# Kernel tuning notes

Hardware: AMD Instinct MI355X
Metric: run time of the kernel (lower is better)

Reference implementation:

```python
import jax, jax.numpy as jnp
import numpy as np

N = 50000      # nodes
E = 800000     # edges
F_IN = 256     # feature_dim
H = 128        # inter_dim
D = 64         # embd_dim
MAX_LOGSTD = 10.0
LEAKY_SLOPE = 0.01


def _lin_params(key, fan_in, fan_out):
    kw, kb = jax.random.split(key)
    s = 1.0 / np.sqrt(fan_in)
    W = jax.random.uniform(kw, (fan_in, fan_out), minval=-s, maxval=s, dtype=jnp.float32)
    b = jax.random.uniform(kb, (fan_out,), minval=-s, maxval=s, dtype=jnp.float32)
    return W, b


def setup_inputs() -> dict:
    key = jax.random.key(0)
    ks = jax.random.split(key, 12)
    x = jax.random.normal(ks[0], (N, F_IN), dtype=jnp.float32)
    edge_index = jax.random.randint(ks[1], (2, E), 0, N, dtype=jnp.int64)
    W_gcn, b_gcn = _lin_params(ks[2], F_IN, H)
    Wq_mu, bq_mu = _lin_params(ks[3], H, D)
    Wk_mu, bk_mu = _lin_params(ks[4], H, D)
    Wv_mu, bv_mu = _lin_params(ks[5], H, D)
    Ws_mu, bs_mu = _lin_params(ks[6], H, D)
    Wq_ls, bq_ls = _lin_params(ks[7], H, D)
    Wk_ls, bk_ls = _lin_params(ks[8], H, D)
    Wv_ls, bv_ls = _lin_params(ks[9], H, D)
    Ws_ls, bs_ls = _lin_params(ks[10], H, D)
    return dict(x=x, edge_index=edge_index, W_gcn=W_gcn, b_gcn=b_gcn,
                Wq_mu=Wq_mu, bq_mu=bq_mu, Wk_mu=Wk_mu, bk_mu=bk_mu,
                Wv_mu=Wv_mu, bv_mu=bv_mu, Ws_mu=Ws_mu, bs_mu=bs_mu,
                Wq_ls=Wq_ls, bq_ls=bq_ls, Wk_ls=Wk_ls, bk_ls=bk_ls,
                Wv_ls=Wv_ls, bv_ls=bv_ls, Ws_ls=Ws_ls, bs_ls=bs_ls)


def gcn_conv(x, src, dst, W, b, n):
    # PyG GCNConv: h = xW; add self loops; norm = d^-1/2[src]*d^-1/2[dst]; scatter-add to dst; + b
    h = x @ W
    loop = jnp.arange(n, dtype=src.dtype)
    src2 = jnp.concatenate([src, loop])
    dst2 = jnp.concatenate([dst, loop])
    deg = jax.ops.segment_sum(jnp.ones_like(dst2, dtype=h.dtype), dst2, num_segments=n)
    dinv = jnp.where(deg > 0, jax.lax.rsqrt(deg), 0.0)
    norm = dinv[src2] * dinv[dst2]                       # [E+N]
    out = jax.ops.segment_sum(h[src2] * norm[:, None], dst2, num_segments=n)
    return out + b


def transformer_conv(x, src, dst, Wq, bq, Wk, bk, Wv, bv, Ws, bs, n):
    # PyG TransformerConv, heads=1, concat=True, beta=False, root_weight=True
    c = Wq.shape[1]
    q = x @ Wq + bq
    k = x @ Wk + bk
    v = x @ Wv + bv
    alpha = jnp.sum(q[dst] * k[src], axis=-1) / jnp.sqrt(jnp.asarray(c, x.dtype))  # [E]
    amax = jax.ops.segment_max(alpha, dst, num_segments=n)
    ex = jnp.exp(alpha - amax[dst])
    denom = jax.ops.segment_sum(ex, dst, num_segments=n)
    w = ex / (denom[dst] + 1e-16)                        # scatter softmax over edges per dst
    out = jax.ops.segment_sum(v[src] * w[:, None], dst, num_segments=n)
    return out + (x @ Ws + bs)


def reference(x, edge_index, W_gcn, b_gcn,
              Wq_mu, bq_mu, Wk_mu, bk_mu, Wv_mu, bv_mu, Ws_mu, bs_mu,
              Wq_ls, bq_ls, Wk_ls, bk_ls, Wv_ls, bv_ls, Ws_ls, bs_ls):
    n = x.shape[0]
    src, dst = edge_index[0], edge_index[1]
    h = gcn_conv(x, src, dst, W_gcn, b_gcn, n)
    h = jnp.where(h >= 0, h, LEAKY_SLOPE * h)            # LeakyReLU(0.01)
    mu = transformer_conv(h, src, dst, Wq_mu, bq_mu, Wk_mu, bk_mu, Wv_mu, bv_mu, Ws_mu, bs_mu, n)
    logstd = transformer_conv(h, src, dst, Wq_ls, bq_ls, Wk_ls, bk_ls, Wv_ls, bv_ls, Ws_ls, bs_ls, n)
    logstd = jnp.minimum(logstd, MAX_LOGSTD)
    return mu, logstd
```

## Files before the change

### kernel.cpp

```cpp
#include <hip/hip_runtime.h>
#include <math.h>

#define N_NODES 50000
#define N_EDGES 800000
#define F_IN    256
#define H_DIM   128
#define D_DIM   64
#define MAX_LOGSTD 10.0f
#define LEAKY_SLOPE 0.01f

#define NB       196
#define BCAP     5000
#define GEMM_BLK 782

using bf16x8 = __attribute__((ext_vector_type(8))) short;
using f32x4  = __attribute__((ext_vector_type(4))) float;

__device__ inline float bflo(unsigned u) { return __uint_as_float(u << 16); }
__device__ inline float bfhi(unsigned u) { return __uint_as_float(u & 0xFFFF0000u); }
__device__ inline unsigned short f2bf(float f) {
    unsigned u = __float_as_uint(f);
    u += 0x7FFFu + ((u >> 16) & 1u);
    return (unsigned short)(u >> 16);
}
__device__ inline unsigned pack2(float a, float b) {
    return (unsigned)f2bf(a) | ((unsigned)f2bf(b) << 16);
}

__global__ void k_prep(const float* __restrict__ Wg,
                       const float* __restrict__ Wq0, const float* __restrict__ Wk0,
                       const float* __restrict__ Wv0, const float* __restrict__ Ws0,
                       const float* __restrict__ Wq1, const float* __restrict__ Wk1,
                       const float* __restrict__ Wv1, const float* __restrict__ Ws1,
                       unsigned short* __restrict__ wfg, unsigned short* __restrict__ wfm,
                       unsigned short* __restrict__ wfl, int* __restrict__ gCursor) {
    int blk = blockIdx.x, t = threadIdx.x;
    if (blk == 384) { if (t < 256) gCursor[t] = 0; return; }
    int grp = blk >> 7;
    int tid = (blk & 127) * 256 + t;
    if (grp == 0) {
        int j = tid & 7, ct = (tid >> 3) & 1, ks = (tid >> 4) & 7;
        int l = (tid >> 7) & 63, w = tid >> 13;
        int k = ks * 32 + (l >> 4) * 8 + j;
        int n = w * 32 + ct * 16 + (l & 15);
        wfg[tid] = f2bf(Wg[k * H_DIM + n]);
    } else {
        int j = tid & 7, ct = (tid >> 3) & 3, ks = (tid >> 5) & 3;
        int l = (tid >> 7) & 63, w = tid >> 13;
        int k = ks * 32 + (l >> 4) * 8 + j;
        int n = ct * 16 + (l & 15);
        const float* Wsrc = (grp == 1)
            ? ((w == 0) ? Wq0 : (w == 1) ? Wk0 : (w == 2) ? Wv0 : Ws0)
            : ((w == 0) ? Wq1 : (w == 1) ? Wk1 : (w == 2) ? Wv1 : Ws1);
        unsigned short val = f2bf(Wsrc[k * D_DIM + n]);
        if (grp == 1) wfm[tid] = val; else wfl[tid] = val;
    }
}

__global__ __launch_bounds__(256) void k_bucketA(
        const int* __restrict__ src, const int* __restrict__ dst,
        int* __restrict__ gCursor, uint2* __restrict__ staging) {
    __shared__ int cnt[NB];
    __shared__ int base[NB];
    int t = threadIdx.x;
    int e0 = blockIdx.x * 4096;
    for (int i = t; i < NB; i += 256) cnt[i] = 0;
    __syncthreads();
    int s[16], d[16], b[16];
#pragma unroll
    for (int i = 0; i < 16; ++i) {
        int e = e0 + t + i * 256;
        if (e < N_EDGES) {
            s[i] = src[e]; d[i] = dst[e]; b[i] = d[i] >> 8;
            atomicAdd(&cnt[b[i]], 1);
        } else b[i] = -1;
    }
    __syncthreads();
    for (int i = t; i < NB; i += 256) base[i] = atomicAdd(&gCursor[i], cnt[i]);
    __syncthreads();
    for (int i = t; i < NB; i += 256) cnt[i] = 0;
    __syncthreads();
#pragma unroll
    for (int i = 0; i < 16; ++i) {
        if (b[i] >= 0) {
            int lp = atomicAdd(&cnt[b[i]], 1);
            staging[(size_t)b[i] * BCAP + base[b[i]] + lp] =
                make_uint2((unsigned)s[i], (unsigned)d[i]);
        }
    }
}

__global__ __launch_bounds__(256) void k_bucketB(
        const uint2* __restrict__ staging, const int* __restrict__ gCursor,
        int* __restrict__ rowptr, float* __restrict__ dinv, int* __restrict__ srcs) {
    __shared__ int sg[256];
    __shared__ int dcnt[256], doff[256], dcur[256];
    int b = blockIdx.x, t = threadIdx.x;
    sg[t] = (t < NB) ? gCursor[t] : 0;
    dcnt[t] = 0;
    __syncthreads();
    int n = sg[b];
    for (int off = 1; off < 256; off <<= 1) {
        int u = (t >= off) ? sg[t - off] : 0;
        __syncthreads();
        sg[t] += u;
        __syncthreads();
    }
    int bb = sg[b] - n;
// ... 47 lines not shown
        float4 a1 = xg[(size_t)grow * 64 + c16 * 2 + 1];
        uint4 o;
        o.x = pack2(a0.x, a0.y); o.y = pack2(a0.z, a0.w);
        o.z = pack2(a1.x, a1.y); o.w = pack2(a1.z, a1.w);
        sA[row * 32 + (c16 ^ (row & 7))] = o;
    }
    __syncthreads();
    f32x4 zero = {0.f, 0.f, 0.f, 0.f};
    f32x4 acc[4][2];
#pragma unroll
    for (int rt = 0; rt < 4; ++rt) { acc[rt][0] = zero; acc[rt][1] = zero; }
    int lr = l & 15, lh = l >> 4;
#pragma unroll
    for (int ks = 0; ks < 8; ++ks) {
        bf16x8 a[4];
#pragma unroll
        for (int rt = 0; rt < 4; ++rt) {
            int row = rt * 16 + lr;
            int c4 = (ks * 4 + lh) ^ (row & 7);
            a[rt] = ((const bf16x8*)sA)[row * 32 + c4];
        }
#pragma unroll
        for (int rt = 0; rt < 4; ++rt) {
            acc[rt][0] = __builtin_amdgcn_mfma_f32_16x16x32_bf16(a[rt], bfr[ks][0], acc[rt][0], 0, 0, 0);
            acc[rt][1] = __builtin_amdgcn_mfma_f32_16x16x32_bf16(a[rt], bfr[ks][1], acc[rt][1], 0, 0, 0);
        }
    }
#pragma unroll
    for (int rt = 0; rt < 4; ++rt)
#pragma unroll
        for (int j = 0; j < 4; ++j) {
            int row = r0 + rt * 16 + lh * 4 + j;
            if (row < N_NODES) {
                float dv = dinv[row];
                size_t base = (size_t)row * H_DIM + w * 32 + lr;
                h0b[base]      = f2bf(acc[rt][0][j] * dv);
                h0b[base + 16] = f2bf(acc[rt][1][j] * dv);
            }
        }
}

__global__ void k_gcn_gather(const unsigned short* __restrict__ h0b,
                             const int* __restrict__ rowptr, const int* __restrict__ srcs,
                             const float* __restrict__ dinv, const float* __restrict__ b,
                             unsigned short* __restrict__ hb) {
    int t = threadIdx.x;
    int node = blockIdx.x * 16 + (t >> 4);
    int sl = t & 15;
    if (node >= N_NODES) return;
    uint4 U = ((const uint4*)(h0b + (size_t)node * H_DIM))[sl];
    float acc[8] = {bflo(U.x), bfhi(U.x), bflo(U.y), bfhi(U.y),
                    bflo(U.z), bfhi(U.z), bflo(U.w), bfhi(U.w)};
    int beg = rowptr[node], end = rowptr[node + 1];
    for (int p = beg; p < end; ++p) {
        int s = srcs[p];
        uint4 V = ((const uint4*)(h0b + (size_t)s * H_DIM))[sl];
        acc[0] += bflo(V.x); acc[1] += bfhi(V.x);
        acc[2] += bflo(V.y); acc[3] += bfhi(V.y);
        acc[4] += bflo(V.z); acc[5] += bfhi(V.z);
        acc[6] += bflo(V.w); acc[7] += bfhi(V.w);
    }
    float dv = dinv[node];
    float out[8];
#pragma unroll
    for (int i = 0; i < 8; ++i) {
        float val = acc[i] * dv + b[sl * 8 + i];
        out[i] = (val >= 0.f) ? val : LEAKY_SLOPE * val;
    }
    uint4 o;
    o.x = pack2(out[0], out[1]); o.y = pack2(out[2], out[3]);
    o.z = pack2(out[4], out[5]); o.w = pack2(out[6], out[7]);
    ((uint4*)(hb + (size_t)node * H_DIM))[sl] = o;
}

__global__ __launch_bounds__(256) void k_qkvs_mfma(
        const unsigned short* __restrict__ hb, const unsigned short* __restrict__ wfrag,
        const float* __restrict__ bq, const float* __restrict__ bk,
        const float* __restrict__ bv, const float* __restrict__ bs,
        float* __restrict__ q, unsigned short* __restrict__ kvb,
        float* __restrict__ outp) {
    __shared__ uint4 sA[64 * 16];
    int t = threadIdx.x, l = t & 63, w = t >> 6;
    int r0 = blockIdx.x * 64;
    const bf16x8* Wf = ((const bf16x8*)wfrag) + ((w * 64 + l) << 4);
    bf16x8 bfr[4][4];
#pragma unroll
    for (int ks = 0; ks < 4; ++ks)
#pragma unroll
        for (int ct = 0; ct < 4; ++ct) bfr[ks][ct] = Wf[ks * 4 + ct];
    const uint4* hg = (const uint4*)hb;
#pragma unroll
    for (int p = 0; p < 4; ++p) {
        int idx = t + p * 256;
        int row = idx >> 4, c16 = idx & 15;
        int grow = min(r0 + row, N_NODES - 1);
        sA[row * 16 + (c16 ^ (row & 7))] = hg[(size_t)grow * 16 + c16];
    }
    __syncthreads();
    f32x4 zero = {0.f, 0.f, 0.f, 0.f};
    f32x4 acc[4][4];
#pragma unroll
    for (int rt = 0; rt < 4; ++rt)
#pragma unroll
        for (int ct = 0; ct < 4; ++ct) acc[rt][ct] = zero;
    int lr = l & 15, lh = l >> 4;
#pragma unroll
    for (int ks = 0; ks < 4; ++ks) {
        bf16x8 a[4];
#pragma unroll
        for (int rt = 0; rt < 4; ++rt) {
            int row = rt * 16 + lr;
            int c4 = (ks * 4 + lh) ^ (row & 7);
            a[rt] = ((const bf16x8*)sA)[row * 16 + c4];
        }
#pragma unroll
        for (int rt = 0; rt < 4; ++rt)
#pragma unroll
            for (int ct = 0; ct < 4; ++ct)
                acc[rt][ct] = __builtin_amdgcn_mfma_f32_16x16x32_bf16(a[rt], bfr[ks][ct], acc[rt][ct], 0, 0, 0);
    }
    const float* bias = (w == 0) ? bq : (w == 1) ? bk : (w == 2) ? bv : bs;
    float bcol[4];
#pragma unroll
    for (int ct = 0; ct < 4; ++ct) bcol[ct] = bias[ct * 16 + lr];
#pragma unroll
    for (int rt = 0; rt < 4; ++rt)
#pragma unroll
        for (int j = 0; j < 4; ++j) {
            int row = r0 + rt * 16 + lh * 4 + j;
            if (row >= N_NODES) continue;
            float v0 = acc[rt][0][j] + bcol[0];
            float v1 = acc[rt][1][j] + bcol[1];
            float v2 = acc[rt][2][j] + bcol[2];
            float v3 = acc[rt][3][j] + bcol[3];
            if (w == 0) {
                float* qp = q + (size_t)row * D_DIM + lr;
                qp[0] = v0; qp[16] = v1; qp[32] = v2; qp[48] = v3;
            } else if (w == 1) {
                unsigned short* kp = kvb + (size_t)row * 128 + lr;
                kp[0] = f2bf(v0); kp[16] = f2bf(v1); kp[32] = f2bf(v2); kp[48] = f2bf(v3);
            } else if (w == 2) {
                unsigned short* vp = kvb + (size_t)row * 128 + 64 + lr;
                vp[0] = f2bf(v0); vp[16] = f2bf(v1); vp[32] = f2bf(v2); vp[48] = f2bf(v3);
            } else {
                float* op = outp + (size_t)row * D_DIM + lr;
                op[0] = v0; op[16] = v1; op[32] = v2; op[48] = v3;
            }
        }
}

__global__ void k_attn2(const float* __restrict__ qm, const float* __restrict__ ql,
                        const unsigned short* __restrict__ kvm, const unsigned short* __restrict__ kvl,
                        const int* __restrict__ rowptr, const int* __restrict__ srcs,
                        float* __restrict__ mu_out, float* __restrict__ ls_out) {
    int t = threadIdx.x;
    int node = blockIdx.x * 4 + (t >> 6);
    if (node >= N_NODES) return;
    int l = t & 63, g = l >> 4, sl = l & 15;
    float4 qm4 = ((const float4*)(qm + (size_t)node * D_DIM))[sl];
    float4 ql4 = ((const float4*)(ql + (size_t)node * D_DIM))[sl];
    qm4.x *= 0.125f; qm4.y *= 0.125f; qm4.z *= 0.125f; qm4.w *= 0.125f;
    ql4.x *= 0.125f; ql4.y *= 0.125f; ql4.z *= 0.125f; ql4.w *= 0.125f;
    int beg = rowptr[node], end = rowptr[node + 1];
    int deg = end - beg;
    int p0 = beg + ((deg * g) >> 2);
    int p1 = beg + ((deg * (g + 1)) >> 2);
    float m_m = -INFINITY, den_m = 0.f;
    float m_l = -INFINITY, den_l = 0.f;
    float4 am = make_float4(0.f, 0.f, 0.f, 0.f);
    float4 al = make_float4(0.f, 0.f, 0.f, 0.f);
    for (int p = p0; p < p1; ++p) {
        int s = srcs[p];
        const unsigned short* km = kvm + (size_t)s * 128;
        const unsigned short* kl = kvl + (size_t)s * 128;
        uint2 kum = *(const uint2*)(km + sl * 4);
        uint2 vum = *(const uint2*)(km + 64 + sl * 4);
        uint2 kul = *(const uint2*)(kl + sl * 4);
        uint2 vul = *(const uint2*)(kl + 64 + sl * 4);
        float dm = qm4.x * bflo(kum.x);
        dm = fmaf(qm4.y, bfhi(kum.x), dm);
        dm = fmaf(qm4.z, bflo(kum.y), dm);
        dm = fmaf(qm4.w, bfhi(kum.y), dm);
        float dl = ql4.x * bflo(kul.x);
        dl = fmaf(ql4.y, bfhi(kul.x), dl);
        dl = fmaf(ql4.z, bflo(kul.y), dl);
        dl = fmaf(ql4.w, bfhi(kul.y), dl);
        dm += __shfl_xor(dm, 1); dm += __shfl_xor(dm, 2);
        dm += __shfl_xor(dm, 4); dm += __shfl_xor(dm, 8);
        dl += __shfl_xor(dl, 1); dl += __shfl_xor(dl, 2);
        dl += __shfl_xor(dl, 4); dl += __shfl_xor(dl, 8);
        if (dm <= m_m) {
            float ex = __expf(dm - m_m);
            den_m += ex;
            am.x = fmaf(ex, bflo(vum.x), am.x);
            am.y = fmaf(ex, bfhi(vum.x), am.y);
            am.z = fmaf(ex, bflo(vum.y), am.z);
            am.w = fmaf(ex, bfhi(vum.y), am.w);
        } else {
            float sc = __expf(m_m - dm);
            den_m = fmaf(den_m, sc, 1.f);
            am.x = fmaf(am.x, sc, bflo(vum.x));
            am.y = fmaf(am.y, sc, bfhi(vum.x));
            am.z = fmaf(am.z, sc, bflo(vum.y));
            am.w = fmaf(am.w, sc, bfhi(vum.y));
            m_m = dm;
        }
        if (dl <= m_l) {
            float ex = __expf(dl - m_l);
            den_l += ex;
            al.x = fmaf(ex, bflo(vul.x), al.x);
            al.y = fmaf(ex, bfhi(vul.x), al.y);
            al.z = fmaf(ex, bflo(vul.y), al.z);
            al.w = fmaf(ex, bfhi(vul.y), al.w);
        } else {
            float sc = __expf(m_l - dl);
            den_l = fmaf(den_l, sc, 1.f);
            al.x = fmaf(al.x, sc, bflo(vul.x));
            al.y = fmaf(al.y, sc, bfhi(vul.x));
            al.z = fmaf(al.z, sc, bflo(vul.y));
            al.w = fmaf(al.w, sc, bfhi(vul.y));
            m_l = dl;
        }
    }
    float M = m_m;
    M = fmaxf(M, __shfl_xor(M, 16)); M = fmaxf(M, __shfl_xor(M, 32));
    float sc = (m_m == -INFINITY) ? 0.f : __expf(m_m - M);
    den_m *= sc; am.x *= sc; am.y *= sc; am.z *= sc; am.w *= sc;
    den_m += __shfl_xor(den_m, 16); den_m += __shfl_xor(den_m, 32);
    am.x += __shfl_xor(am.x, 16); am.x += __shfl_xor(am.x, 32);
    am.y += __shfl_xor(am.y, 16); am.y += __shfl_xor(am.y, 32);
    am.z += __shfl_xor(am.z, 16); am.z += __shfl_xor(am.z, 32);
    am.w += __shfl_xor(am.w, 16); am.w += __shfl_xor(am.w, 32);

    float L = m_l;
    L = fmaxf(L, __shfl_xor(L, 16)); L = fmaxf(L, __shfl_xor(L, 32));
    float scl = (m_l == -INFINITY) ? 0.f : __expf(m_l - L);
    den_l *= scl; al.x *= scl; al.y *= scl; al.z *= scl; al.w *= scl;
    den_l += __shfl_xor(den_l, 16); den_l += __shfl_xor(den_l, 32);
    al.x += __shfl_xor(al.x, 16); al.x += __shfl_xor(al.x, 32);
    al.y += __shfl_xor(al.y, 16); al.y += __shfl_xor(al.y, 32);
    al.z += __shfl_xor(al.z, 16); al.z += __shfl_xor(al.z, 32);
    al.w += __shfl_xor(al.w, 16); al.w += __shfl_xor(al.w, 32);

    if (g == 0) {
        float inv = 1.f / (den_m + 1e-16f);
        float4 sk = ((float4*)mu_out)[node * 16 + sl];
        float4 o = make_float4(am.x * inv + sk.x, am.y * inv + sk.y,
                               am.z * inv + sk.z, am.w * inv + sk.w);
        ((float4*)mu_out)[node * 16 + sl] = o;
        float invl = 1.f / (den_l + 1e-16f);
        float4 skl = ((float4*)ls_out)[node * 16 + sl];
        float4 ol = make_float4(al.x * invl + skl.x, al.y * invl + skl.y,
                                al.z * invl + skl.z, al.w * invl + skl.w);
        ol.x = fminf(ol.x, MAX_LOGSTD); ol.y = fminf(ol.y, MAX_LOGSTD);
        ol.z = fminf(ol.z, MAX_LOGSTD); ol.w = fminf(ol.w, MAX_LOGSTD);
        ((float4*)ls_out)[node * 16 + sl] = ol;
    }
}

extern "C" void kernel_launch(void* const* d_in, const int* in_sizes, int n_in,
                              void* d_out, int out_size, void* d_ws, size_t ws_size,
                              hipStream_t stream) {
    const float* x     = (const float*)d_in[0];
    const int*   ei    = (const int*)d_in[1];
    const int*   src   = ei;
    const int*   dst   = ei + N_EDGES;
    const float* W_gcn = (const float*)d_in[2];
    const float* b_gcn = (const float*)d_in[3];
    const float* Wm[8]; const float* Wl8[8];
    for (int i = 0; i < 8; ++i) { Wm[i] = (const float*)d_in[4 + i]; Wl8[i] = (const float*)d_in[12 + i]; }

    float* out    = (float*)d_out;
    float* mu_out = out;
    float* ls_out = out + N_NODES * D_DIM;

    float* ws   = (float*)d_ws;
    float* q_l  = ws;
    float* dinv = q_l + (size_t)N_NODES * D_DIM;
    unsigned short* kvm = (unsigned short*)(dinv + N_NODES);
    unsigned short* h0b = kvm + (size_t)N_NODES * H_DIM;
    unsigned short* hb  = h0b + (size_t)N_NODES * H_DIM;
    unsigned short* wfg = hb + (size_t)N_NODES * H_DIM;
    unsigned short* wfm = wfg + 32768;
    unsigned short* wfl = wfm + 32768;
    int* rowptr  = (int*)(wfl + 32768);
    int* srcs    = rowptr + N_NODES + 4;
    int* gCursor = srcs + N_EDGES;
    uint2* staging = (uint2*)(gCursor + 256);
    float* q_m     = (float*)staging;

    const int B = 256;
    k_prep<<<385, B, 0, stream>>>(W_gcn, Wm[0], Wm[2], Wm[4], Wm[6],
                                  Wl8[0], Wl8[2], Wl8[4], Wl8[6],
                                  wfg, wfm, wfl, gCursor);
    k_bucketA<<<(N_EDGES + 4095) / 4096, B, 0, stream>>>(src, dst, gCursor, staging);
    k_bucketB<<<NB, B, 0, stream>>>(staging, gCursor, rowptr, dinv, srcs);

    k_gemm_gcn_mfma<<<GEMM_BLK, B, 0, stream>>>(x, wfg, dinv, h0b);
    k_gcn_gather<<<(N_NODES + 15) / 16, B, 0, stream>>>(h0b, rowptr, srcs, dinv, b_gcn, hb);

    unsigned short* kvl = h0b;
    k_qkvs_mfma<<<GEMM_BLK, B, 0, stream>>>(hb, wfm, Wm[1], Wm[3], Wm[5], Wm[7],
                                            q_m, kvm, mu_out);
    k_qkvs_mfma<<<GEMM_BLK, B, 0, stream>>>(hb, wfl, Wl8[1], Wl8[3], Wl8[5], Wl8[7],
                                            q_l, kvl, ls_out);
    k_attn2<<<(N_NODES + 3) / 4, B, 0, stream>>>(q_m, q_l, kvm, kvl, rowptr, srcs,
                                                 mu_out, ls_out);
}
```

Baseline: 226.6 us.

## Fuse mu/logstd QKVS GEMMs into one launch and unroll gather loops by two

The two per-conv QKVS MFMA GEMM launches become a single 512-thread kernel. Its eight waves cover both convolutions, so each 64-row tile of h is loaded into shared memory once instead of twice. The GCN gather loop and the attention edge loop are unrolled by two so that more independent gather loads are in flight per iteration. The cost is higher register pressure in the attention kernel and larger blocks in the fused GEMM.

```diff
diff --git a/kernel.cpp b/kernel.cpp
--- a/kernel.cpp
+++ b/kernel.cpp
@@ -25,6 +25,36 @@
 }
 __device__ inline unsigned pack2(float a, float b) {
     return (unsigned)f2bf(a) | ((unsigned)f2bf(b) << 16);
+}
+__device__ inline float dot4(const float4& q, uint2 ku) {
+    float d = q.x * bflo(ku.x);
+    d = fmaf(q.y, bfhi(ku.x), d);
+    d = fmaf(q.z, bflo(ku.y), d);
+    d = fmaf(q.w, bfhi(ku.y), d);
+    return d;
+}
+__device__ inline float red16(float d) {
+    d += __shfl_xor(d, 1); d += __shfl_xor(d, 2);
+    d += __shfl_xor(d, 4); d += __shfl_xor(d, 8);
+    return d;
+}
+__device__ inline void sm_step(float d, uint2 vu, float& m, float& den, float4& a) {
+    if (d <= m) {
+        float ex = __expf(d - m);
+        den += ex;
+        a.x = fmaf(ex, bflo(vu.x), a.x);
+        a.y = fmaf(ex, bfhi(vu.x), a.y);
+        a.z = fmaf(ex, bflo(vu.y), a.z);
+        a.w = fmaf(ex, bfhi(vu.y), a.w);
+    } else {
+        float sc = __expf(m - d);
+        den = fmaf(den, sc, 1.f);
+        a.x = fmaf(a.x, sc, bflo(vu.x));
+        a.y = fmaf(a.y, sc, bfhi(vu.x));
+        a.z = fmaf(a.z, sc, bflo(vu.y));
+        a.w = fmaf(a.w, sc, bfhi(vu.y));
+        m = d;
+    }
 }
 
 __global__ void k_prep(const float* __restrict__ Wg,
@@ -207,7 +237,21 @@
     float acc[8] = {bflo(U.x), bfhi(U.x), bflo(U.y), bfhi(U.y),
                     bflo(U.z), bfhi(U.z), bflo(U.w), bfhi(U.w)};
     int beg = rowptr[node], end = rowptr[node + 1];
-    for (int p = beg; p < end; ++p) {
+    int p = beg;
+    for (; p + 1 < end; p += 2) {
+        int s0 = srcs[p], s1 = srcs[p + 1];
+        uint4 V0 = ((const uint4*)(h0b + (size_t)s0 * H_DIM))[sl];
+        uint4 V1 = ((const uint4*)(h0b + (size_t)s1 * H_DIM))[sl];
+        acc[0] += bflo(V0.x); acc[1] += bfhi(V0.x);
+        acc[2] += bflo(V0.y); acc[3] += bfhi(V0.y);
+        acc[4] += bflo(V0.z); acc[5] += bfhi(V0.z);
+        acc[6] += bflo(V0.w); acc[7] += bfhi(V0.w);
+        acc[0] += bflo(V1.x); acc[1] += bfhi(V1.x);
+        acc[2] += bflo(V1.y); acc[3] += bfhi(V1.y);
+        acc[4] += bflo(V1.z); acc[5] += bfhi(V1.z);
+        acc[6] += bflo(V1.w); acc[7] += bfhi(V1.w);
+    }
+    if (p < end) {
         int s = srcs[p];
         uint4 V = ((const uint4*)(h0b + (size_t)s * H_DIM))[sl];
         acc[0] += bflo(V.x); acc[1] += bfhi(V.x);
@@ -228,16 +272,21 @@
     ((uint4*)(hb + (size_t)node * H_DIM))[sl] = o;
 }
 
-__global__ __launch_bounds__(256) void k_qkvs_mfma(
-        const unsigned short* __restrict__ hb, const unsigned short* __restrict__ wfrag,
-        const float* __restrict__ bq, const float* __restrict__ bk,
-        const float* __restrict__ bv, const float* __restrict__ bs,
-        float* __restrict__ q, unsigned short* __restrict__ kvb,
-        float* __restrict__ outp) {
+__global__ __launch_bounds__(512) void k_qkvs2_mfma(
+        const unsigned short* __restrict__ hb,
+        const unsigned short* __restrict__ wfm, const unsigned short* __restrict__ wfl,
+        const float* __restrict__ bq0, const float* __restrict__ bk0,
+        const float* __restrict__ bv0, const float* __restrict__ bs0,
+        const float* __restrict__ bq1, const float* __restrict__ bk1,
+        const float* __restrict__ bv1, const float* __restrict__ bs1,
+        float* __restrict__ qm, unsigned short* __restrict__ kvm, float* __restrict__ mu_out,
+        float* __restrict__ ql, unsigned short* __restrict__ kvl, float* __restrict__ ls_out) {
     __shared__ uint4 sA[64 * 16];
     int t = threadIdx.x, l = t & 63, w = t >> 6;
+    int conv = w >> 2, role = w & 3;
     int r0 = blockIdx.x * 64;
-    const bf16x8* Wf = ((const bf16x8*)wfrag) + ((w * 64 + l) << 4);
+    const unsigned short* wfrag = conv ? wfl : wfm;
+    const bf16x8* Wf = ((const bf16x8*)wfrag) + ((role * 64 + l) << 4);
     bf16x8 bfr[4][4];
 #pragma unroll
     for (int ks = 0; ks < 4; ++ks)
@@ -245,8 +294,8 @@
         for (int ct = 0; ct < 4; ++ct) bfr[ks][ct] = Wf[ks * 4 + ct];
     const uint4* hg = (const uint4*)hb;
 #pragma unroll
-    for (int p = 0; p < 4; ++p) {
-        int idx = t + p * 256;
+    for (int p = 0; p < 2; ++p) {
+        int idx = t + p * 512;
         int row = idx >> 4, c16 = idx & 15;
         int grow = min(r0 + row, N_NODES - 1);
         sA[row * 16 + (c16 ^ (row & 7))] = hg[(size_t)grow * 16 + c16];
@@ -274,7 +323,12 @@
             for (int ct = 0; ct < 4; ++ct)
                 acc[rt][ct] = __builtin_amdgcn_mfma_f32_16x16x32_bf16(a[rt], bfr[ks][ct], acc[rt][ct], 0, 0, 0);
     }
-    const float* bias = (w == 0) ? bq : (w == 1) ? bk : (w == 2) ? bv : bs;
+    const float* bias = conv
+        ? ((role == 0) ? bq1 : (role == 1) ? bk1 : (role == 2) ? bv1 : bs1)
+        : ((role == 0) ? bq0 : (role == 1) ? bk0 : (role == 2) ? bv0 : bs0);
+    float* qp_   = conv ? ql : qm;
+    unsigned short* kvp_ = conv ? kvl : kvm;
+    float* op_   = conv ? ls_out : mu_out;
     float bcol[4];
 #pragma unroll
     for (int ct = 0; ct < 4; ++ct) bcol[ct] = bias[ct * 16 + lr];
@@ -288,17 +342,17 @@
             float v1 = acc[rt][1][j] + bcol[1];
             float v2 = acc[rt][2][j] + bcol[2];
             float v3 = acc[rt][3][j] + bcol[3];
-            if (w == 0) {
-                float* qp = q + (size_t)row * D_DIM + lr;
+            if (role == 0) {
+                float* qp = qp_ + (size_t)row * D_DIM + lr;
                 qp[0] = v0; qp[16] = v1; qp[32] = v2; qp[48] = v3;
-            } else if (w == 1) {
-                unsigned short* kp = kvb + (size_t)row * 128 + lr;
+            } else if (role == 1) {
+                unsigned short* kp = kvp_ + (size_t)row * 128 + lr;
                 kp[0] = f2bf(v0); kp[16] = f2bf(v1); kp[32] = f2bf(v2); kp[48] = f2bf(v3);
-            } else if (w == 2) {
-                unsigned short* vp = kvb + (size_t)row * 128 + 64 + lr;
+            } else if (role == 2) {
+                unsigned short* vp = kvp_ + (size_t)row * 128 + 64 + lr;
                 vp[0] = f2bf(v0); vp[16] = f2bf(v1); vp[32] = f2bf(v2); vp[48] = f2bf(v3);
             } else {
-                float* op = outp + (size_t)row * D_DIM + lr;
+                float* op = op_ + (size_t)row * D_DIM + lr;
                 op[0] = v0; op[16] = v1; op[32] = v2; op[48] = v3;
             }
         }
@@ -324,7 +378,31 @@
     float m_l = -INFINITY, den_l = 0.f;
     float4 am = make_float4(0.f, 0.f, 0.f, 0.f);
     float4 al = make_float4(0.f, 0.f, 0.f, 0.f);
-    for (int p = p0; p < p1; ++p) {
+    int p = p0;
+    for (; p + 1 < p1; p += 2) {
+        int s0 = srcs[p], s1 = srcs[p + 1];
+        const unsigned short* km0 = kvm + (size_t)s0 * 128;
+        const unsigned short* kl0 = kvl + (size_t)s0 * 128;
+        const unsigned short* km1 = kvm + (size_t)s1 * 128;
+        const unsigned short* kl1 = kvl + (size_t)s1 * 128;
+        uint2 kum0 = *(const uint2*)(km0 + sl * 4);
+        uint2 vum0 = *(const uint2*)(km0 + 64 + sl * 4);
+        uint2 kul0 = *(const uint2*)(kl0 + sl * 4);
+        uint2 vul0 = *(const uint2*)(kl0 + 64 + sl * 4);
+        uint2 kum1 = *(const uint2*)(km1 + sl * 4);
+        uint2 vum1 = *(const uint2*)(km1 + 64 + sl * 4);
+        uint2 kul1 = *(const uint2*)(kl1 + sl * 4);
+        uint2 vul1 = *(const uint2*)(kl1 + 64 + sl * 4);
+        float dm0 = red16(dot4(qm4, kum0));
+        float dl0 = red16(dot4(ql4, kul0));
+        float dm1 = red16(dot4(qm4, kum1));
+        float dl1 = red16(dot4(ql4, kul1));
+        sm_step(dm0, vum0, m_m, den_m, am);
+        sm_step(dm1, vum1, m_m, den_m, am);
+        sm_step(dl0, vul0, m_l, den_l, al);
+        sm_step(dl1, vul1, m_l, den_l, al);
+    }
+    if (p < p1) {
         int s = srcs[p];
         const unsigned short* km = kvm + (size_t)s * 128;
         const unsigned short* kl = kvl + (size_t)s * 128;
@@ -332,50 +410,10 @@
         uint2 vum = *(const uint2*)(km + 64 + sl * 4);
         uint2 kul = *(const uint2*)(kl + sl * 4);
         uint2 vul = *(const uint2*)(kl + 64 + sl * 4);
-        float dm = qm4.x * bflo(kum.x);
-        dm = fmaf(qm4.y, bfhi(kum.x), dm);
-        dm = fmaf(qm4.z, bflo(kum.y), dm);
-        dm = fmaf(qm4.w, bfhi(kum.y), dm);
-        float dl = ql4.x * bflo(kul.x);
-        dl = fmaf(ql4.y, bfhi(kul.x), dl);
-        dl = fmaf(ql4.z, bflo(kul.y), dl);
-        dl = fmaf(ql4.w, bfhi(kul.y), dl);
-        dm += __shfl_xor(dm, 1); dm += __shfl_xor(dm, 2);
-        dm += __shfl_xor(dm, 4); dm += __shfl_xor(dm, 8);
-        dl += __shfl_xor(dl, 1); dl += __shfl_xor(dl, 2);
-        dl += __shfl_xor(dl, 4); dl += __shfl_xor(dl, 8);
-        if (dm <= m_m) {
-            float ex = __expf(dm - m_m);
-            den_m += ex;
-            am.x = fmaf(ex, bflo(vum.x), am.x);
-            am.y = fmaf(ex, bfhi(vum.x), am.y);
-            am.z = fmaf(ex, bflo(vum.y), am.z);
-            am.w = fmaf(ex, bfhi(vum.y), am.w);
-        } else {
-            float sc = __expf(m_m - dm);
-            den_m = fmaf(den_m, sc, 1.f);
-            am.x = fmaf(am.x, sc, bflo(vum.x));
-            am.y = fmaf(am.y, sc, bfhi(vum.x));
-            am.z = fmaf(am.z, sc, bflo(vum.y));
-            am.w = fmaf(am.w, sc, bfhi(vum.y));
-            m_m = dm;
-        }
-        if (dl <= m_l) {
-            float ex = __expf(dl - m_l);
-            den_l += ex;
-            al.x = fmaf(ex, bflo(vul.x), al.x);
-            al.y = fmaf(ex, bfhi(vul.x), al.y);
-            al.z = fmaf(ex, bflo(vul.y), al.z);
-            al.w = fmaf(ex, bfhi(vul.y), al.w);
-        } else {
-            float sc = __expf(m_l - dl);
-            den_l = fmaf(den_l, sc, 1.f);
-            al.x = fmaf(al.x, sc, bflo(vul.x));
-            al.y = fmaf(al.y, sc, bfhi(vul.x));
-            al.z = fmaf(al.z, sc, bflo(vul.y));
-            al.w = fmaf(al.w, sc, bfhi(vul.y));
-            m_l = dl;
-        }
+        float dm = red16(dot4(qm4, kum));
+        float dl = red16(dot4(ql4, kul));
+        sm_step(dm, vum, m_m, den_m, am);
+        sm_step(dl, vul, m_l, den_l, al);
     }
     float M = m_m;
     M = fmaxf(M, __shfl_xor(M, 16)); M = fmaxf(M, __shfl_xor(M, 32));
@@ -455,10 +493,11 @@
     k_gcn_gather<<<(N_NODES + 15) / 16, B, 0, stream>>>(h0b, rowptr, srcs, dinv, b_gcn, hb);
 
     unsigned short* kvl = h0b;
-    k_qkvs_mfma<<<GEMM_BLK, B, 0, stream>>>(hb, wfm, Wm[1], Wm[3], Wm[5], Wm[7],
-                                            q_m, kvm, mu_out);
-    k_qkvs_mfma<<<GEMM_BLK, B, 0, stream>>>(hb, wfl, Wl8[1], Wl8[3], Wl8[5], Wl8[7],
-                                            q_l, kvl, ls_out);
+    k_qkvs2_mfma<<<GEMM_BLK, 512, 0, stream>>>(hb, wfm, wfl,
+                                               Wm[1], Wm[3], Wm[5], Wm[7],
+                                               Wl8[1], Wl8[3], Wl8[5], Wl8[7],
+                                               q_m, kvm, mu_out,
+                                               q_l, kvl, ls_out);
     k_attn2<<<(N_NODES + 3) / 4, B, 0, stream>>>(q_m, q_l, kvm, kvl, rowptr, srcs,
                                                  mu_out, ls_out);
 }
```

After: 210.6 us. -7.0%, faster.

## Fold Q·K and V projections into attention via precomputed Wq·Wkᵀ and post-aggregation projection

Applied to the files above, without the earlier changes.

The attention score q·k is rewritten as h_dst·(Wq Wkᵀ)·h_src plus a bias term, so the kernel gathers the shared 128-dim bf16 h rows once for both convolutions instead of separate per-conv K/V buffers. Softmax-weighted h sums are written out and then projected by Wv in a new MFMA kernel, with bv added only for nodes that have edges. A fused kernel computes the transformed queries and skip projections for both convs. The GCN gather loop is also unrolled by two. The aim is to cut gather bandwidth and the K/V GEMM work, at the cost of an extra kernel, 128-wide queries and some extra bf16 rounding.

```diff
diff --git a/kernel.cpp b/kernel.cpp
--- a/kernel.cpp
+++ b/kernel.cpp
@@ -26,34 +26,79 @@
 __device__ inline unsigned pack2(float a, float b) {
     return (unsigned)f2bf(a) | ((unsigned)f2bf(b) << 16);
 }
-
-__global__ void k_prep(const float* __restrict__ Wg,
-                       const float* __restrict__ Wq0, const float* __restrict__ Wk0,
-                       const float* __restrict__ Wv0, const float* __restrict__ Ws0,
-                       const float* __restrict__ Wq1, const float* __restrict__ Wk1,
-                       const float* __restrict__ Wv1, const float* __restrict__ Ws1,
-                       unsigned short* __restrict__ wfg, unsigned short* __restrict__ wfm,
-                       unsigned short* __restrict__ wfl, int* __restrict__ gCursor) {
+__device__ inline float red16(float d) {
+    d += __shfl_xor(d, 1); d += __shfl_xor(d, 2);
+    d += __shfl_xor(d, 4); d += __shfl_xor(d, 8);
+    return d;
+}
+
+__global__ void k_prepM(const float* __restrict__ Wq0, const float* __restrict__ Wk0,
+                        const float* __restrict__ bq0,
+                        const float* __restrict__ Wq1, const float* __restrict__ Wk1,
+                        const float* __restrict__ bq1,
+                        float* __restrict__ Mf, float* __restrict__ bpm,
+                        float* __restrict__ bpl) {
+    int blk = blockIdx.x, t = threadIdx.x;
+    if (blk < 128) {
+        int tid = blk * 256 + t;
+        int conv = tid >> 14;
+        int rem = tid & 16383;
+        int i = rem >> 7, jj = rem & 127;
+        const float* Wq = conv ? Wq1 : Wq0;
+        const float* Wk = conv ? Wk1 : Wk0;
+        float s = 0.f;
+#pragma unroll 8
+        for (int n = 0; n < 64; ++n) s = fmaf(Wq[i * 64 + n], Wk[jj * 64 + n], s);
+        Mf[conv * 16384 + i * 128 + jj] = s * 0.125f;
+    } else {
+        int jj = t & 127;
+        int conv = t >> 7;
+        const float* Wk = conv ? Wk1 : Wk0;
+        const float* bq = conv ? bq1 : bq0;
+        float s = 0.f;
+#pragma unroll 8
+        for (int n = 0; n < 64; ++n) s = fmaf(bq[n], Wk[jj * 64 + n], s);
+        if (conv) bpl[jj] = s * 0.125f; else bpm[jj] = s * 0.125f;
+    }
+}
+
+__global__ void k_prep(const float* __restrict__ Wg, const float* __restrict__ Mf,
+                       const float* __restrict__ Ws0, const float* __restrict__ Ws1,
+                       const float* __restrict__ Wv0, const float* __restrict__ Wv1,
+                       unsigned short* __restrict__ wfg, unsigned short* __restrict__ wfp,
+                       unsigned short* __restrict__ wfv, int* __restrict__ gCursor) {
     int blk = blockIdx.x, t = threadIdx.x;
     if (blk == 384) { if (t < 256) gCursor[t] = 0; return; }
-    int grp = blk >> 7;
-    int tid = (blk & 127) * 256 + t;
-    if (grp == 0) {
+    if (blk < 128) {
+        int tid = blk * 256 + t;
         int j = tid & 7, ct = (tid >> 3) & 1, ks = (tid >> 4) & 7;
         int l = (tid >> 7) & 63, w = tid >> 13;
         int k = ks * 32 + (l >> 4) * 8 + j;
         int n = w * 32 + ct * 16 + (l & 15);
         wfg[tid] = f2bf(Wg[k * H_DIM + n]);
-    } else {
+    } else if (blk < 320) {
+        int tid = (blk - 128) * 256 + t;
         int j = tid & 7, ct = (tid >> 3) & 3, ks = (tid >> 5) & 3;
         int l = (tid >> 7) & 63, w = tid >> 13;
         int k = ks * 32 + (l >> 4) * 8 + j;
         int n = ct * 16 + (l & 15);
-        const float* Wsrc = (grp == 1)
-            ? ((w == 0) ? Wq0 : (w == 1) ? Wk0 : (w == 2) ? Wv0 : Ws0)
-            : ((w == 0) ? Wq1 : (w == 1) ? Wk1 : (w == 2) ? Wv1 : Ws1);
-        unsigned short val = f2bf(Wsrc[k * D_DIM + n]);
-        if (grp == 1) wfm[tid] = val; else wfl[tid] = val;
+        float val;
+        if (w == 2)      val = Ws0[k * D_DIM + n];
+        else if (w == 5) val = Ws1[k * D_DIM + n];
+        else {
+            int conv = (w >= 3);
+            int half = conv ? (w - 3) : w;
+            val = Mf[conv * 16384 + k * 128 + half * 64 + n];
+        }
+        wfp[tid] = f2bf(val);
+    } else {
+        int tid = (blk - 320) * 256 + t;
+        int j = tid & 7, ct = (tid >> 3) & 3, ks = (tid >> 5) & 3;
+        int l = (tid >> 7) & 63, w = tid >> 13;
+        int k = ks * 32 + (l >> 4) * 8 + j;
+        int n = ct * 16 + (l & 15);
+        const float* Wv = w ? Wv1 : Wv0;
+        wfv[tid] = f2bf(Wv[k * D_DIM + n]);
     }
 }
 
@@ -207,7 +252,21 @@
     float acc[8] = {bflo(U.x), bfhi(U.x), bflo(U.y), bfhi(U.y),
                     bflo(U.z), bfhi(U.z), bflo(U.w), bfhi(U.w)};
     int beg = rowptr[node], end = rowptr[node + 1];
-    for (int p = beg; p < end; ++p) {
+    int p = beg;
+    for (; p + 1 < end; p += 2) {
+        int s0 = srcs[p], s1 = srcs[p + 1];
+        uint4 V0 = ((const uint4*)(h0b + (size_t)s0 * H_DIM))[sl];
+        uint4 V1 = ((const uint4*)(h0b + (size_t)s1 * H_DIM))[sl];
+        acc[0] += bflo(V0.x); acc[1] += bfhi(V0.x);
+        acc[2] += bflo(V0.y); acc[3] += bfhi(V0.y);
+        acc[4] += bflo(V0.z); acc[5] += bfhi(V0.z);
+        acc[6] += bflo(V0.w); acc[7] += bfhi(V0.w);
+        acc[0] += bflo(V1.x); acc[1] += bfhi(V1.x);
+        acc[2] += bflo(V1.y); acc[3] += bfhi(V1.y);
+        acc[4] += bflo(V1.z); acc[5] += bfhi(V1.z);
+        acc[6] += bflo(V1.w); acc[7] += bfhi(V1.w);
+    }
+    if (p < end) {
         int s = srcs[p];
         uint4 V = ((const uint4*)(h0b + (size_t)s * H_DIM))[sl];
         acc[0] += bflo(V.x); acc[1] += bfhi(V.x);
@@ -228,16 +287,16 @@
     ((uint4*)(hb + (size_t)node * H_DIM))[sl] = o;
 }
 
-__global__ __launch_bounds__(256) void k_qkvs_mfma(
-        const unsigned short* __restrict__ hb, const unsigned short* __restrict__ wfrag,
-        const float* __restrict__ bq, const float* __restrict__ bk,
-        const float* __restrict__ bv, const float* __restrict__ bs,
-        float* __restrict__ q, unsigned short* __restrict__ kvb,
-        float* __restrict__ outp) {
+__global__ __launch_bounds__(384) void k_qs_mfma(
+        const unsigned short* __restrict__ hb, const unsigned short* __restrict__ wfp,
+        const float* __restrict__ bpm, const float* __restrict__ bpl,
+        const float* __restrict__ bs0, const float* __restrict__ bs1,
+        unsigned short* __restrict__ qmb, unsigned short* __restrict__ qlb,
+        float* __restrict__ mu_out, float* __restrict__ ls_out) {
     __shared__ uint4 sA[64 * 16];
     int t = threadIdx.x, l = t & 63, w = t >> 6;
     int r0 = blockIdx.x * 64;
-    const bf16x8* Wf = ((const bf16x8*)wfrag) + ((w * 64 + l) << 4);
+    const bf16x8* Wf = ((const bf16x8*)wfp) + ((w * 64 + l) << 4);
     bf16x8 bfr[4][4];
 #pragma unroll
     for (int ks = 0; ks < 4; ++ks)
@@ -245,11 +304,13 @@
         for (int ct = 0; ct < 4; ++ct) bfr[ks][ct] = Wf[ks * 4 + ct];
     const uint4* hg = (const uint4*)hb;
 #pragma unroll
-    for (int p = 0; p < 4; ++p) {
-        int idx = t + p * 256;
-        int row = idx >> 4, c16 = idx & 15;
-        int grow = min(r0 + row, N_NODES - 1);
-        sA[row * 16 + (c16 ^ (row & 7))] = hg[(size_t)grow * 16 + c16];
+    for (int p = 0; p < 3; ++p) {
+        int idx = t + p * 384;
+        if (idx < 1024) {
+            int row = idx >> 4, c16 = idx & 15;
+            int grow = min(r0 + row, N_NODES - 1);
+            sA[row * 16 + (c16 ^ (row & 7))] = hg[(size_t)grow * 16 + c16];
+        }
     }
     __syncthreads();
     f32x4 zero = {0.f, 0.f, 0.f, 0.f};
@@ -274,143 +335,221 @@
             for (int ct = 0; ct < 4; ++ct)
                 acc[rt][ct] = __builtin_amdgcn_mfma_f32_16x16x32_bf16(a[rt], bfr[ks][ct], acc[rt][ct], 0, 0, 0);
     }
-    const float* bias = (w == 0) ? bq : (w == 1) ? bk : (w == 2) ? bv : bs;
-    float bcol[4];
-#pragma unroll
-    for (int ct = 0; ct < 4; ++ct) bcol[ct] = bias[ct * 16 + lr];
-#pragma unroll
-    for (int rt = 0; rt < 4; ++rt)
-#pragma unroll
-        for (int j = 0; j < 4; ++j) {
-            int row = r0 + rt * 16 + lh * 4 + j;
-            if (row >= N_NODES) continue;
-            float v0 = acc[rt][0][j] + bcol[0];
-            float v1 = acc[rt][1][j] + bcol[1];
-            float v2 = acc[rt][2][j] + bcol[2];
-            float v3 = acc[rt][3][j] + bcol[3];
-            if (w == 0) {
-                float* qp = q + (size_t)row * D_DIM + lr;
-                qp[0] = v0; qp[16] = v1; qp[32] = v2; qp[48] = v3;
-            } else if (w == 1) {
-                unsigned short* kp = kvb + (size_t)row * 128 + lr;
-                kp[0] = f2bf(v0); kp[16] = f2bf(v1); kp[32] = f2bf(v2); kp[48] = f2bf(v3);
-            } else if (w == 2) {
-                unsigned short* vp = kvb + (size_t)row * 128 + 64 + lr;
-                vp[0] = f2bf(v0); vp[16] = f2bf(v1); vp[32] = f2bf(v2); vp[48] = f2bf(v3);
-            } else {
-                float* op = outp + (size_t)row * D_DIM + lr;
-                op[0] = v0; op[16] = v1; op[32] = v2; op[48] = v3;
+    if (w == 2 || w == 5) {
+        const float* bias = (w == 2) ? bs0 : bs1;
+        float* op_ = (w == 2) ? mu_out : ls_out;
+        float bcol[4];
+#pragma unroll
+        for (int ct = 0; ct < 4; ++ct) bcol[ct] = bias[ct * 16 + lr];
+#pragma unroll
+        for (int rt = 0; rt < 4; ++rt)
+#pragma unroll
+            for (int j = 0; j < 4; ++j) {
+                int row = r0 + rt * 16 + lh * 4 + j;
+                if (row >= N_NODES) continue;
+                float* op = op_ + (size_t)row * D_DIM + lr;
+                op[0]  = acc[rt][0][j] + bcol[0];
+                op[16] = acc[rt][1][j] + bcol[1];
+                op[32] = acc[rt][2][j] + bcol[2];
+                op[48] = acc[rt][3][j] + bcol[3];
             }
-        }
-}
-
-__global__ void k_attn2(const float* __restrict__ qm, const float* __restrict__ ql,
-                        const unsigned short* __restrict__ kvm, const unsigned short* __restrict__ kvl,
+    } else {
+        int conv = (w >= 3);
+        int half = conv ? (w - 3) : w;
+        const float* bp = conv ? bpl : bpm;
+        unsigned short* qb = conv ? qlb : qmb;
+        float bcol[4];
+#pragma unroll
+        for (int ct = 0; ct < 4; ++ct) bcol[ct] = bp[half * 64 + ct * 16 + lr];
+#pragma unroll
+        for (int rt = 0; rt < 4; ++rt)
+#pragma unroll
+            for (int j = 0; j < 4; ++j) {
+                int row = r0 + rt * 16 + lh * 4 + j;
+                if (row >= N_NODES) continue;
+                unsigned short* qp = qb + (size_t)row * 128 + half * 64 + lr;
+                qp[0]  = f2bf(acc[rt][0][j] + bcol[0]);
+                qp[16] = f2bf(acc[rt][1][j] + bcol[1]);
+                qp[32] = f2bf(acc[rt][2][j] + bcol[2]);
+                qp[48] = f2bf(acc[rt][3][j] + bcol[3]);
+            }
+    }
+}
+
+__global__ void k_attn3(const unsigned short* __restrict__ qmb,
+                        const unsigned short* __restrict__ qlb,
+                        const unsigned short* __restrict__ hb,
                         const int* __restrict__ rowptr, const int* __restrict__ srcs,
-                        float* __restrict__ mu_out, float* __restrict__ ls_out) {
+                        unsigned short* __restrict__ Sbm, unsigned short* __restrict__ Sbl) {
     int t = threadIdx.x;
     int node = blockIdx.x * 4 + (t >> 6);
     if (node >= N_NODES) return;
     int l = t & 63, g = l >> 4, sl = l & 15;
-    float4 qm4 = ((const float4*)(qm + (size_t)node * D_DIM))[sl];
-    float4 ql4 = ((const float4*)(ql + (size_t)node * D_DIM))[sl];
-    qm4.x *= 0.125f; qm4.y *= 0.125f; qm4.z *= 0.125f; qm4.w *= 0.125f;
-    ql4.x *= 0.125f; ql4.y *= 0.125f; ql4.z *= 0.125f; ql4.w *= 0.125f;
+    uint4 qmu = ((const uint4*)(qmb + (size_t)node * 128))[sl];
+    uint4 qlu = ((const uint4*)(qlb + (size_t)node * 128))[sl];
+    float qm8[8] = {bflo(qmu.x), bfhi(qmu.x), bflo(qmu.y), bfhi(qmu.y),
+                    bflo(qmu.z), bfhi(qmu.z), bflo(qmu.w), bfhi(qmu.w)};
+    float ql8[8] = {bflo(qlu.x), bfhi(qlu.x), bflo(qlu.y), bfhi(qlu.y),
+                    bflo(qlu.z), bfhi(qlu.z), bflo(qlu.w), bfhi(qlu.w)};
     int beg = rowptr[node], end = rowptr[node + 1];
     int deg = end - beg;
     int p0 = beg + ((deg * g) >> 2);
     int p1 = beg + ((deg * (g + 1)) >> 2);
     float m_m = -INFINITY, den_m = 0.f;
     float m_l = -INFINITY, den_l = 0.f;
-    float4 am = make_float4(0.f, 0.f, 0.f, 0.f);
-    float4 al = make_float4(0.f, 0.f, 0.f, 0.f);
+    float Sm[8] = {0.f, 0.f, 0.f, 0.f, 0.f, 0.f, 0.f, 0.f};
+    float Sl[8] = {0.f, 0.f, 0.f, 0.f, 0.f, 0.f, 0.f, 0.f};
     for (int p = p0; p < p1; ++p) {
         int s = srcs[p];
-        const unsigned short* km = kvm + (size_t)s * 128;
-        const unsigned short* kl = kvl + (size_t)s * 128;
-        uint2 kum = *(const uint2*)(km + sl * 4);
-        uint2 vum = *(const uint2*)(km + 64 + sl * 4);
-        uint2 kul = *(const uint2*)(kl + sl * 4);
-        uint2 vul = *(const uint2*)(kl + 64 + sl * 4);
-        float dm = qm4.x * bflo(kum.x);
-        dm = fmaf(qm4.y, bfhi(kum.x), dm);
-        dm = fmaf(qm4.z, bflo(kum.y), dm);
-        dm = fmaf(qm4.w, bfhi(kum.y), dm);
-        float dl = ql4.x * bflo(kul.x);
-        dl = fmaf(ql4.y, bfhi(kul.x), dl);
-        dl = fmaf(ql4.z, bflo(kul.y), dl);
-        dl = fmaf(ql4.w, bfhi(kul.y), dl);
-        dm += __shfl_xor(dm, 1); dm += __shfl_xor(dm, 2);
-        dm += __shfl_xor(dm, 4); dm += __shfl_xor(dm, 8);
-        dl += __shfl_xor(dl, 1); dl += __shfl_xor(dl, 2);
-        dl += __shfl_xor(dl, 4); dl += __shfl_xor(dl, 8);
+        uint4 hu = ((const uint4*)(hb + (size_t)s * 128))[sl];
+        float h8[8] = {bflo(hu.x), bfhi(hu.x), bflo(hu.y), bfhi(hu.y),
+                       bflo(hu.z), bfhi(hu.z), bflo(hu.w), bfhi(hu.w)};
+        float dm = 0.f, dl = 0.f;
+#pragma unroll
+        for (int i = 0; i < 8; ++i) {
+            dm = fmaf(qm8[i], h8[i], dm);
+            dl = fmaf(ql8[i], h8[i], dl);
+        }
+        dm = red16(dm);
+        dl = red16(dl);
         if (dm <= m_m) {
             float ex = __expf(dm - m_m);
             den_m += ex;
-            am.x = fmaf(ex, bflo(vum.x), am.x);
-            am.y = fmaf(ex, bfhi(vum.x), am.y);
-            am.z = fmaf(ex, bflo(vum.y), am.z);
-            am.w = fmaf(ex, bfhi(vum.y), am.w);
+#pragma unroll
+            for (int i = 0; i < 8; ++i) Sm[i] = fmaf(ex, h8[i], Sm[i]);
         } else {
             float sc = __expf(m_m - dm);
             den_m = fmaf(den_m, sc, 1.f);
-            am.x = fmaf(am.x, sc, bflo(vum.x));
-            am.y = fmaf(am.y, sc, bfhi(vum.x));
-            am.z = fmaf(am.z, sc, bflo(vum.y));
-            am.w = fmaf(am.w, sc, bfhi(vum.y));
+#pragma unroll
+            for (int i = 0; i < 8; ++i) Sm[i] = fmaf(Sm[i], sc, h8[i]);
             m_m = dm;
         }
         if (dl <= m_l) {
             float ex = __expf(dl - m_l);
             den_l += ex;
-            al.x = fmaf(ex, bflo(vul.x), al.x);
-            al.y = fmaf(ex, bfhi(vul.x), al.y);
-            al.z = fmaf(ex, bflo(vul.y), al.z);
-            al.w = fmaf(ex, bfhi(vul.y), al.w);
+#pragma unroll
+            for (int i = 0; i < 8; ++i) Sl[i] = fmaf(ex, h8[i], Sl[i]);
         } else {
             float sc = __expf(m_l - dl);
             den_l = fmaf(den_l, sc, 1.f);
-            al.x = fmaf(al.x, sc, bflo(vul.x));
-            al.y = fmaf(al.y, sc, bfhi(vul.x));
-            al.z = fmaf(al.z, sc, bflo(vul.y));
-            al.w = fmaf(al.w, sc, bfhi(vul.y));
+#pragma unroll
+            for (int i = 0; i < 8; ++i) Sl[i] = fmaf(Sl[i], sc, h8[i]);
             m_l = dl;
         }
     }
     float M = m_m;
     M = fmaxf(M, __shfl_xor(M, 16)); M = fmaxf(M, __shfl_xor(M, 32));
     float sc = (m_m == -INFINITY) ? 0.f : __expf(m_m - M);
-    den_m *= sc; am.x *= sc; am.y *= sc; am.z *= sc; am.w *= sc;
+    den_m *= sc;
+#pragma unroll
+    for (int i = 0; i < 8; ++i) Sm[i] *= sc;
     den_m += __shfl_xor(den_m, 16); den_m += __shfl_xor(den_m, 32);
-    am.x += __shfl_xor(am.x, 16); am.x += __shfl_xor(am.x, 32);
-    am.y += __shfl_xor(am.y, 16); am.y += __shfl_xor(am.y, 32);
-    am.z += __shfl_xor(am.z, 16); am.z += __shfl_xor(am.z, 32);
-    am.w += __shfl_xor(am.w, 16); am.w += __shfl_xor(am.w, 32);
-
+#pragma unroll
+    for (int i = 0; i < 8; ++i) {
+        Sm[i] += __shfl_xor(Sm[i], 16);
+        Sm[i] += __shfl_xor(Sm[i], 32);
+    }
     float L = m_l;
     L = fmaxf(L, __shfl_xor(L, 16)); L = fmaxf(L, __shfl_xor(L, 32));
     float scl = (m_l == -INFINITY) ? 0.f : __expf(m_l - L);
-    den_l *= scl; al.x *= scl; al.y *= scl; al.z *= scl; al.w *= scl;
+    den_l *= scl;
+#pragma unroll
+    for (int i = 0; i < 8; ++i) Sl[i] *= scl;
     den_l += __shfl_xor(den_l, 16); den_l += __shfl_xor(den_l, 32);
-    al.x += __shfl_xor(al.x, 16); al.x += __shfl_xor(al.x, 32);
-    al.y += __shfl_xor(al.y, 16); al.y += __shfl_xor(al.y, 32);
-    al.z += __shfl_xor(al.z, 16); al.z += __shfl_xor(al.z, 32);
-    al.w += __shfl_xor(al.w, 16); al.w += __shfl_xor(al.w, 32);
-
+#pragma unroll
+    for (int i = 0; i < 8; ++i) {
+        Sl[i] += __shfl_xor(Sl[i], 16);
+        Sl[i] += __shfl_xor(Sl[i], 32);
+    }
     if (g == 0) {
         float inv = 1.f / (den_m + 1e-16f);
-        float4 sk = ((float4*)mu_out)[node * 16 + sl];
-        float4 o = make_float4(am.x * inv + sk.x, am.y * inv + sk.y,
-                               am.z * inv + sk.z, am.w * inv + sk.w);
-        ((float4*)mu_out)[node * 16 + sl] = o;
+        uint4 o;
+        o.x = pack2(Sm[0] * inv, Sm[1] * inv);
+        o.y = pack2(Sm[2] * inv, Sm[3] * inv);
+        o.z = pack2(Sm[4] * inv, Sm[5] * inv);
+        o.w = pack2(Sm[6] * inv, Sm[7] * inv);
+        ((uint4*)Sbm)[(size_t)node * 16 + sl] = o;
         float invl = 1.f / (den_l + 1e-16f);
-        float4 skl = ((float4*)ls_out)[node * 16 + sl];
-        float4 ol = make_float4(al.x * invl + skl.x, al.y * invl + skl.y,
-                                al.z * invl + skl.z, al.w * invl + skl.w);
-        ol.x = fminf(ol.x, MAX_LOGSTD); ol.y = fminf(ol.y, MAX_LOGSTD);
-        ol.z = fminf(ol.z, MAX_LOGSTD); ol.w = fminf(ol.w, MAX_LOGSTD);
-        ((float4*)ls_out)[node * 16 + sl] = ol;
-    }
+        uint4 ol;
+        ol.x = pack2(Sl[0] * invl, Sl[1] * invl);
+        ol.y = pack2(Sl[2] * invl, Sl[3] * invl);
+        ol.z = pack2(Sl[4] * invl, Sl[5] * invl);
+        ol.w = pack2(Sl[6] * invl, Sl[7] * invl);
+        ((uint4*)Sbl)[(size_t)node * 16 + sl] = ol;
+    }
+}
+
+__global__ __launch_bounds__(256) void k_proj(
+        const unsigned short* __restrict__ Sbm, const unsigned short* __restrict__ Sbl,
+        const unsigned short* __restrict__ wfv,
+        const float* __restrict__ bv0, const float* __restrict__ bv1,
+        const int* __restrict__ rowptr,
+        float* __restrict__ mu_out, float* __restrict__ ls_out) {
+    __shared__ uint4 sA[2 * 64 * 16];
+    int t = threadIdx.x, l = t & 63, w = t >> 6;
+    int conv = w & 1, rh = w >> 1;
+    int r0 = blockIdx.x * 64;
+    const bf16x8* Wf = ((const bf16x8*)wfv) + ((conv * 64 + l) << 4);
+    bf16x8 bfr[4][4];
+#pragma unroll
+    for (int ks = 0; ks < 4; ++ks)
+#pragma unroll
+        for (int ct = 0; ct < 4; ++ct) bfr[ks][ct] = Wf[ks * 4 + ct];
+#pragma unroll
+    for (int p = 0; p < 8; ++p) {
+        int idx = t + p * 256;
+        int buf = idx >> 10, rem = idx & 1023;
+        int row = rem >> 4, c16 = rem & 15;
+        int grow = min(r0 + row, N_NODES - 1);
+        const uint4* srcp = (const uint4*)(buf ? Sbl : Sbm);
+        sA[buf * 1024 + row * 16 + (c16 ^ (row & 7))] = srcp[(size_t)grow * 16 + c16];
+    }
+    __syncthreads();
+    f32x4 zero = {0.f, 0.f, 0.f, 0.f};
+    f32x4 acc[2][4];
+#pragma unroll
+    for (int rt = 0; rt < 2; ++rt)
+#pragma unroll
+        for (int ct = 0; ct < 4; ++ct) acc[rt][ct] = zero;
+    int lr = l & 15, lh = l >> 4;
+#pragma unroll
+    for (int ks = 0; ks < 4; ++ks) {
+        bf16x8 a[2];
+#pragma unroll
+        for (int rt = 0; rt < 2; ++rt) {
+            int row = rh * 32 + rt * 16 + lr;
+            int c4 = (ks * 4 + lh) ^ (row & 7);
+            a[rt] = ((const bf16x8*)sA)[conv * 1024 + row * 16 + c4];
+        }
+#pragma unroll
+        for (int rt = 0; rt < 2; ++rt)
+#pragma unroll
+            for (int ct = 0; ct < 4; ++ct)
+                acc[rt][ct] = __builtin_amdgcn_mfma_f32_16x16x32_bf16(a[rt], bfr[ks][ct], acc[rt][ct], 0, 0, 0);
+    }
+    const float* bv = conv ? bv1 : bv0;
+    float* ob = conv ? ls_out : mu_out;
+    float bcol[4];
+#pragma unroll
+    for (int ct = 0; ct < 4; ++ct) bcol[ct] = bv[ct * 16 + lr];
+#pragma unroll
+    for (int rt = 0; rt < 2; ++rt)
+#pragma unroll
+        for (int j = 0; j < 4; ++j) {
+            int row = r0 + rh * 32 + rt * 16 + lh * 4 + j;
+            if (row >= N_NODES) continue;
+            float wsum = (rowptr[row + 1] > rowptr[row]) ? 1.f : 0.f;
+            float* op = ob + (size_t)row * D_DIM + lr;
+            float v0 = acc[rt][0][j] + bcol[0] * wsum + op[0];
+            float v1 = acc[rt][1][j] + bcol[1] * wsum + op[16];
+            float v2 = acc[rt][2][j] + bcol[2] * wsum + op[32];
+            float v3 = acc[rt][3][j] + bcol[3] * wsum + op[48];
+            if (conv) {
+                v0 = fminf(v0, MAX_LOGSTD); v1 = fminf(v1, MAX_LOGSTD);
+                v2 = fminf(v2, MAX_LOGSTD); v3 = fminf(v3, MAX_LOGSTD);
+            }
+            op[0] = v0; op[16] = v1; op[32] = v2; op[48] = v3;
+        }
 }
 
 extern "C" void kernel_launch(void* const* d_in, const int* in_sizes, int n_in,
@@ -430,35 +569,38 @@
     float* ls_out = out + N_NODES * D_DIM;
 
     float* ws   = (float*)d_ws;
-    float* q_l  = ws;
-    float* dinv = q_l + (size_t)N_NODES * D_DIM;
-    unsigned short* kvm = (unsigned short*)(dinv + N_NODES);
-    unsigned short* h0b = kvm + (size_t)N_NODES * H_DIM;
-    unsigned short* hb  = h0b + (size_t)N_NODES * H_DIM;
-    unsigned short* wfg = hb + (size_t)N_NODES * H_DIM;
-    unsigned short* wfm = wfg + 32768;
-    unsigned short* wfl = wfm + 32768;
-    int* rowptr  = (int*)(wfl + 32768);
+    float* dinv = ws;
+    float* Mf   = dinv + N_NODES;
+    float* bpm  = Mf + 32768;
+    float* bpl  = bpm + 128;
+    unsigned short* hb  = (unsigned short*)(bpl + 128);
+    unsigned short* h0b = hb + (size_t)N_NODES * H_DIM;
+    unsigned short* qmb = h0b + (size_t)N_NODES * H_DIM;
+    unsigned short* qlb = qmb + (size_t)N_NODES * H_DIM;
+    unsigned short* Sbl = qlb + (size_t)N_NODES * H_DIM;
+    unsigned short* wfg = Sbl + (size_t)N_NODES * H_DIM;
+    unsigned short* wfp = wfg + 32768;
+    unsigned short* wfv = wfp + 49152;
+    int* rowptr  = (int*)(wfv + 16384);
     int* srcs    = rowptr + N_NODES + 4;
     int* gCursor = srcs + N_EDGES;
-    uint2* staging = (uint2*)(gCursor + 256);
-    float* q_m     = (float*)staging;
+    uint2* staging = (uint2*)qmb;
+    unsigned short* Sbm = h0b;
 
     const int B = 256;
-    k_prep<<<385, B, 0, stream>>>(W_gcn, Wm[0], Wm[2], Wm[4], Wm[6],
-                                  Wl8[0], Wl8[2], Wl8[4], Wl8[6],
-                                  wfg, wfm, wfl, gCursor);
+    k_prepM<<<129, B, 0, stream>>>(Wm[0], Wm[2], Wm[1], Wl8[0], Wl8[2], Wl8[1],
+                                   Mf, bpm, bpl);
+    k_prep<<<385, B, 0, stream>>>(W_gcn, Mf, Wm[6], Wl8[6], Wm[4], Wl8[4],
+                                  wfg, wfp, wfv, gCursor);
     k_bucketA<<<(N_EDGES + 4095) / 4096, B, 0, stream>>>(src, dst, gCursor, staging);
     k_bucketB<<<NB, B, 0, stream>>>(staging, gCursor, rowptr, dinv, srcs);
 
     k_gemm_gcn_mfma<<<GEMM_BLK, B, 0, stream>>>(x, wfg, dinv, h0b);
     k_gcn_gather<<<(N_NODES + 15) / 16, B, 0, stream>>>(h0b, rowptr, srcs, dinv, b_gcn, hb);
 
-    unsigned short* kvl = h0b;
-    k_qkvs_mfma<<<GEMM_BLK, B, 0, stream>>>(hb, wfm, Wm[1], Wm[3], Wm[5], Wm[7],
-                                            q_m, kvm, mu_out);
-    k_qkvs_mfma<<<GEMM_BLK, B, 0, stream>>>(hb, wfl, Wl8[1], Wl8[3], Wl8[5], Wl8[7],
-                                            q_l, kvl, ls_out);
-    k_attn2<<<(N_NODES + 3) / 4, B, 0, stream>>>(q_m, q_l, kvm, kvl, rowptr, srcs,
-                                                 mu_out, ls_out);
-}
+    k_qs_mfma<<<GEMM_BLK, 384, 0, stream>>>(hb, wfp, bpm, bpl, Wm[7], Wl8[7],
+                                            qmb, qlb, mu_out, ls_out);
+    k_attn3<<<(N_NODES + 3) / 4, B, 0, stream>>>(qmb, qlb, hb, rowptr, srcs, Sbm, Sbl);
+    k_proj<<<GEMM_BLK, B, 0, stream>>>(Sbm, Sbl, wfv, Wm[5], Wl8[5], rowptr,
+                                       mu_out, ls_out);
+}
```

Result: faster. 201.8 us (-11.0%).
